# Optimization experiments

Hardware: AMD Instinct MI355X
Metric: run time of the kernel (lower is better)

The kernel has to match this reference:

```python
import jax, jax.numpy as jnp
import numpy as np

N, F, O, E = 2048, 128, 128, 16


def setup_inputs() -> dict:
    key = jax.random.key(0)
    ks = jax.random.split(key, 6)
    x = jax.random.normal(ks[0], (N, F), dtype=jnp.float32)
    # two supports (normalized adjacency-like dense matrices)
    support = jax.random.uniform(ks[1], (2, N, N), dtype=jnp.float32)
    edge_feature = jax.random.normal(ks[2], (N, N, E), dtype=jnp.float32)
    # glorot-ish scale for edge weight and dense weights
    weight_edge = jax.random.normal(ks[3], (N, N, E), dtype=jnp.float32) * 0.05
    bias_edge = jnp.zeros((N, N), dtype=jnp.float32)
    glorot = float(np.sqrt(6.0 / (F + O)))
    w0 = jax.random.uniform(ks[4], (F, O), dtype=jnp.float32, minval=-glorot, maxval=glorot)
    w1 = jax.random.uniform(ks[5], (F, O), dtype=jnp.float32, minval=-glorot, maxval=glorot)
    b = jnp.zeros((O,), dtype=jnp.float32)
    return {"x": x, "support": support, "edge_feature": edge_feature,
            "weight_edge": weight_edge, "bias_edge": bias_edge,
            "w0": w0, "w1": w1, "b": b}


def reference(x, support, edge_feature, weight_edge, bias_edge, w0, w1, b):
    # support branch 0: plain GCN propagation  (SpMM expressed dense)
    pre0 = x @ w0                      # [N, O]
    s0 = support[0] @ pre0             # [N, O]
    # support branch 1: edge-feature gated propagation
    pre1 = x @ w1                      # [N, O]
    # per-pair dot of edge features with per-pair weights -> [N, N] gate
    edge = jax.nn.sigmoid(jnp.einsum('nme,nme->nm', edge_feature, weight_edge) + bias_edge)
    s1 = (edge * support[1]) @ pre1    # gated adjacency matmul, [N, O]
    out = s0 + s1 + b                  # add_n + bias
    return jax.nn.relu(out)
```

## Files before the change

kernel.cpp:

```cpp
#include <hip/hip_runtime.h>
#include <math.h>

#define N 2048
#define F 128
#define O 128
#define E 16

typedef __attribute__((ext_vector_type(8))) short          shortx8;
typedef __attribute__((ext_vector_type(8))) unsigned short u16x8;
typedef __attribute__((ext_vector_type(4))) unsigned short u16x4;
typedef __attribute__((ext_vector_type(4))) float          floatx4;

static __device__ __forceinline__ unsigned short f2bf(float f) {
    unsigned int u = __float_as_uint(f);
    unsigned int r = (u + 0x7FFFu + ((u >> 16) & 1u)) >> 16;
    return (unsigned short)r;
}

__global__ __launch_bounds__(256)
void pre_t(const float* __restrict__ x,
           const float* __restrict__ w0,
           const float* __restrict__ w1,
           unsigned short* __restrict__ preT) {
    __shared__ unsigned short wT[128 * 136];
    const int t  = threadIdx.x;
    const int n0 = blockIdx.x * 16;
    const int b  = blockIdx.y;
    const float* __restrict__ wsrc = b ? w1 : w0;

#pragma unroll
    for (int i = 0; i < 64; ++i) {
        const int idx = i * 256 + t;
        const int k = idx >> 7, o = idx & 127;
        wT[o * 136 + k] = f2bf(wsrc[idx]);
    }
    __syncthreads();

    const int lane = t & 63;
    const int wv   = t >> 6;
    const int row  = lane & 15;
    const int kg   = lane >> 4;
    const int col0 = wv * 32 + row;

    floatx4 acc0 = {0.f, 0.f, 0.f, 0.f};
    floatx4 acc1 = {0.f, 0.f, 0.f, 0.f};

#pragma unroll
    for (int kk = 0; kk < 4; ++kk) {
        const float* xp = x + (size_t)(n0 + row) * F + kk * 32 + kg * 8;
        const float4 f0 = *(const float4*)(xp);
        const float4 f1 = *(const float4*)(xp + 4);
        shortx8 a;
        a[0] = (short)f2bf(f0.x); a[1] = (short)f2bf(f0.y);
        a[2] = (short)f2bf(f0.z); a[3] = (short)f2bf(f0.w);
        a[4] = (short)f2bf(f1.x); a[5] = (short)f2bf(f1.y);
        a[6] = (short)f2bf(f1.z); a[7] = (short)f2bf(f1.w);
        const shortx8 bA = *(const shortx8*)(wT + col0 * 136 + kk * 32 + kg * 8);
        const shortx8 bB = *(const shortx8*)(wT + (col0 + 16) * 136 + kk * 32 + kg * 8);
        acc0 = __builtin_amdgcn_mfma_f32_16x16x32_bf16(a, bA, acc0, 0, 0, 0);
        acc1 = __builtin_amdgcn_mfma_f32_16x16x32_bf16(a, bB, acc1, 0, 0, 0);
    }

    const int prow = kg * 4;
    u16x4 s0, s1;
#pragma unroll
    for (int j = 0; j < 4; ++j) { s0[j] = f2bf(acc0[j]); s1[j] = f2bf(acc1[j]); }
    *(u16x4*)(preT + ((size_t)b * O + col0) * N + n0 + prow)      = s0;
    *(u16x4*)(preT + ((size_t)b * O + col0 + 16) * N + n0 + prow) = s1;
}

__global__ __launch_bounds__(256)
void gate_kernel(const float* __restrict__ ef,
                 const float* __restrict__ we,
                 const float* __restrict__ be,
                 const float* __restrict__ sup1,
                 unsigned short* __restrict__ G) {
    const size_t tid  = (size_t)blockIdx.x * 256 + threadIdx.x;
    const size_t pair = tid >> 2;
    const int    sub  = (int)(threadIdx.x & 3);
    const float4 e4 = ((const float4*)ef)[pair * 4 + sub];
    const float4 w4 = ((const float4*)we)[pair * 4 + sub];
    float v = e4.x * w4.x + e4.y * w4.y + e4.z * w4.z + e4.w * w4.w;
    v += __shfl_xor(v, 1);
    v += __shfl_xor(v, 2);
    if (sub == 0) {
        const float t = v + be[pair];
        const float g = (1.f / (1.f + __expf(-t))) * sup1[pair];
        G[pair] = f2bf(g);
    }
}

__global__ __launch_bounds__(512, 4)
void gemm_direct(const float* __restrict__ S0,
                 const unsigned short* __restrict__ G,
                 const unsigned short* __restrict__ preT,
                 const float* __restrict__ bias,
                 float* __restrict__ out) {
    __shared__ float red[8][16][36];

    const int bx   = blockIdx.x;
    const int orig = (bx & 7) * 64 + (bx >> 3);
    const int rb   = orig >> 2;
    const int cg   = orig & 3;
    const int n0   = rb * 16;

    const int t    = threadIdx.x;
    const int lane = t & 63;
    const int wv   = t >> 6;
    const int m_b  = wv * 256;
    const int row  = lane & 15;
    const int kg   = lane >> 4;
    const int col0 = cg * 32 + row;

    const float*          aS = S0   + (size_t)(n0 + row) * N + m_b + kg * 8;
    const unsigned short* aG = G    + (size_t)(n0 + row) * N + m_b + kg * 8;
    const unsigned short* b0 = preT + (size_t)col0 * N        + m_b + kg * 8;
    const unsigned short* b1 = b0 + (size_t)16 * N;
    const unsigned short* c0 = b0 + (size_t)O * N;
    const unsigned short* c1 = b1 + (size_t)O * N;

    floatx4 acc0 = {0.f, 0.f, 0.f, 0.f};
    floatx4 acc1 = {0.f, 0.f, 0.f, 0.f};

#pragma unroll 2
    for (int s = 0; s < 8; ++s) {
        const int mo = s * 32;
        const float4 f0 = *(const float4*)(aS + mo);
        const float4 f1 = *(const float4*)(aS + mo + 4);
        const shortx8 a_g = *(const shortx8*)(aG + mo);
        const shortx8 b00 = *(const shortx8*)(b0 + mo);
        const shortx8 b01 = *(const shortx8*)(b1 + mo);
        const shortx8 b10 = *(const shortx8*)(c0 + mo);
        const shortx8 b11 = *(const shortx8*)(c1 + mo);
        shortx8 a_s;
        a_s[0] = (short)f2bf(f0.x); a_s[1] = (short)f2bf(f0.y);
        a_s[2] = (short)f2bf(f0.z); a_s[3] = (short)f2bf(f0.w);
        a_s[4] = (short)f2bf(f1.x); a_s[5] = (short)f2bf(f1.y);
        a_s[6] = (short)f2bf(f1.z); a_s[7] = (short)f2bf(f1.w);
        acc0 = __builtin_amdgcn_mfma_f32_16x16x32_bf16(a_s, b00, acc0, 0, 0, 0);
        acc0 = __builtin_amdgcn_mfma_f32_16x16x32_bf16(a_g, b10, acc0, 0, 0, 0);
        acc1 = __builtin_amdgcn_mfma_f32_16x16x32_bf16(a_s, b01, acc1, 0, 0, 0);
        acc1 = __builtin_amdgcn_mfma_f32_16x16x32_bf16(a_g, b11, acc1, 0, 0, 0);
    }

    const int prow = kg * 4;
#pragma unroll
    for (int j = 0; j < 4; ++j) {
        red[wv][prow + j][row]      = acc0[j];
        red[wv][prow + j][16 + row] = acc1[j];
    }
    __syncthreads();

    if (t < 256) {
        const int r = t >> 4;
        const int c = (t & 15) * 2;
        float v0 = 0.f, v1 = 0.f;
#pragma unroll
        for (int w = 0; w < 8; ++w) {
            v0 += red[w][r][c];
            v1 += red[w][r][c + 1];
        }
        v0 = fmaxf(v0 + bias[cg * 32 + c],     0.f);
        v1 = fmaxf(v1 + bias[cg * 32 + c + 1], 0.f);
        float2 o2; o2.x = v0; o2.y = v1;
        *(float2*)(out + (size_t)(n0 + r) * O + cg * 32 + c) = o2;
    }
}

extern "C" void kernel_launch(void* const* d_in, const int* in_sizes, int n_in,
                              void* d_out, int out_size, void* d_ws, size_t ws_size,
                              hipStream_t stream) {
    const float* x   = (const float*)d_in[0];
    const float* sup = (const float*)d_in[1];
    const float* ef  = (const float*)d_in[2];
    const float* we  = (const float*)d_in[3];
    const float* be  = (const float*)d_in[4];
    const float* w0  = (const float*)d_in[5];
    const float* w1  = (const float*)d_in[6];
    const float* b   = (const float*)d_in[7];
    float* out = (float*)d_out;

    unsigned short* preT = (unsigned short*)d_ws;
    unsigned short* G    = preT + 2 * (size_t)N * O;

    pre_t<<<dim3(N / 16, 2), 256, 0, stream>>>(x, w0, w1, preT);
    gate_kernel<<<(unsigned)((size_t)N * N * 4 / 256), 256, 0, stream>>>(
        ef, we, be, sup + (size_t)N * N, G);
    gemm_direct<<<512, 512, 0, stream>>>(sup, G, preT, b, out);
}
```

Before: 130.5 us.

## Pre-convert support0 to bf16 in gate kernel and widen GEMM to 16 waves

The gate kernel now also converts support[0] to bf16 into a workspace buffer, so the final GEMM reads half the bytes for that operand and skips in-loop conversion. The GEMM block doubles to 1024 threads, each wave covering a shorter K slice with all operand loads issued before the MFMAs. This adds an extra fp32 read and bf16 write in the bandwidth-bound gate kernel and a larger shared reduction.

```diff
diff --git a/kernel.cpp b/kernel.cpp
--- a/kernel.cpp
+++ b/kernel.cpp
@@ -74,7 +74,9 @@
                  const float* __restrict__ we,
                  const float* __restrict__ be,
                  const float* __restrict__ sup1,
-                 unsigned short* __restrict__ G) {
+                 const float* __restrict__ S0,
+                 unsigned short* __restrict__ G,
+                 unsigned short* __restrict__ S0bf) {
     const size_t tid  = (size_t)blockIdx.x * 256 + threadIdx.x;
     const size_t pair = tid >> 2;
     const int    sub  = (int)(threadIdx.x & 3);
@@ -87,16 +89,18 @@
         const float t = v + be[pair];
         const float g = (1.f / (1.f + __expf(-t))) * sup1[pair];
         G[pair] = f2bf(g);
+    } else if (sub == 1) {
+        S0bf[pair] = f2bf(S0[pair]);
     }
 }
 
-__global__ __launch_bounds__(512, 4)
-void gemm_direct(const float* __restrict__ S0,
+__global__ __launch_bounds__(1024, 4)
+void gemm_direct(const unsigned short* __restrict__ S0bf,
                  const unsigned short* __restrict__ G,
                  const unsigned short* __restrict__ preT,
                  const float* __restrict__ bias,
                  float* __restrict__ out) {
-    __shared__ float red[8][16][36];
+    __shared__ float red[16][16][36];
 
     const int bx   = blockIdx.x;
     const int orig = (bx & 7) * 64 + (bx >> 3);
@@ -107,40 +111,38 @@
     const int t    = threadIdx.x;
     const int lane = t & 63;
     const int wv   = t >> 6;
-    const int m_b  = wv * 256;
+    const int m_b  = wv * 128;
     const int row  = lane & 15;
     const int kg   = lane >> 4;
     const int col0 = cg * 32 + row;
 
-    const float*          aS = S0   + (size_t)(n0 + row) * N + m_b + kg * 8;
+    const unsigned short* aS = S0bf + (size_t)(n0 + row) * N + m_b + kg * 8;
     const unsigned short* aG = G    + (size_t)(n0 + row) * N + m_b + kg * 8;
     const unsigned short* b0 = preT + (size_t)col0 * N        + m_b + kg * 8;
     const unsigned short* b1 = b0 + (size_t)16 * N;
     const unsigned short* c0 = b0 + (size_t)O * N;
     const unsigned short* c1 = b1 + (size_t)O * N;
 
+    shortx8 As[4], Ag[4], B00[4], B01[4], B10[4], B11[4];
+#pragma unroll
+    for (int s = 0; s < 4; ++s) {
+        const int mo = s * 32;
+        As[s]  = *(const shortx8*)(aS + mo);
+        Ag[s]  = *(const shortx8*)(aG + mo);
+        B00[s] = *(const shortx8*)(b0 + mo);
+        B01[s] = *(const shortx8*)(b1 + mo);
+        B10[s] = *(const shortx8*)(c0 + mo);
+        B11[s] = *(const shortx8*)(c1 + mo);
+    }
+
     floatx4 acc0 = {0.f, 0.f, 0.f, 0.f};
     floatx4 acc1 = {0.f, 0.f, 0.f, 0.f};
-
-#pragma unroll 2
-    for (int s = 0; s < 8; ++s) {
-        const int mo = s * 32;
-        const float4 f0 = *(const float4*)(aS + mo);
-        const float4 f1 = *(const float4*)(aS + mo + 4);
-        const shortx8 a_g = *(const shortx8*)(aG + mo);
-        const shortx8 b00 = *(const shortx8*)(b0 + mo);
-        const shortx8 b01 = *(const shortx8*)(b1 + mo);
-        const shortx8 b10 = *(const shortx8*)(c0 + mo);
-        const shortx8 b11 = *(const shortx8*)(c1 + mo);
-        shortx8 a_s;
-        a_s[0] = (short)f2bf(f0.x); a_s[1] = (short)f2bf(f0.y);
-        a_s[2] = (short)f2bf(f0.z); a_s[3] = (short)f2bf(f0.w);
-        a_s[4] = (short)f2bf(f1.x); a_s[5] = (short)f2bf(f1.y);
-        a_s[6] = (short)f2bf(f1.z); a_s[7] = (short)f2bf(f1.w);
-        acc0 = __builtin_amdgcn_mfma_f32_16x16x32_bf16(a_s, b00, acc0, 0, 0, 0);
-        acc0 = __builtin_amdgcn_mfma_f32_16x16x32_bf16(a_g, b10, acc0, 0, 0, 0);
-        acc1 = __builtin_amdgcn_mfma_f32_16x16x32_bf16(a_s, b01, acc1, 0, 0, 0);
-        acc1 = __builtin_amdgcn_mfma_f32_16x16x32_bf16(a_g, b11, acc1, 0, 0, 0);
+#pragma unroll
+    for (int s = 0; s < 4; ++s) {
+        acc0 = __builtin_amdgcn_mfma_f32_16x16x32_bf16(As[s], B00[s], acc0, 0, 0, 0);
+        acc0 = __builtin_amdgcn_mfma_f32_16x16x32_bf16(Ag[s], B10[s], acc0, 0, 0, 0);
+        acc1 = __builtin_amdgcn_mfma_f32_16x16x32_bf16(As[s], B01[s], acc1, 0, 0, 0);
+        acc1 = __builtin_amdgcn_mfma_f32_16x16x32_bf16(Ag[s], B11[s], acc1, 0, 0, 0);
     }
 
     const int prow = kg * 4;
@@ -156,7 +158,7 @@
         const int c = (t & 15) * 2;
         float v0 = 0.f, v1 = 0.f;
 #pragma unroll
-        for (int w = 0; w < 8; ++w) {
+        for (int w = 0; w < 16; ++w) {
             v0 += red[w][r][c];
             v1 += red[w][r][c + 1];
         }
@@ -182,9 +184,10 @@
 
     unsigned short* preT = (unsigned short*)d_ws;
     unsigned short* G    = preT + 2 * (size_t)N * O;
+    unsigned short* S0bf = G + (size_t)N * N;
 
     pre_t<<<dim3(N / 16, 2), 256, 0, stream>>>(x, w0, w1, preT);
     gate_kernel<<<(unsigned)((size_t)N * N * 4 / 256), 256, 0, stream>>>(
-        ef, we, be, sup + (size_t)N * N, G);
-    gemm_direct<<<512, 512, 0, stream>>>(sup, G, preT, b, out);
+        ef, we, be, sup + (size_t)N * N, sup, G, S0bf);
+    gemm_direct<<<512, 1024, 0, stream>>>(S0bf, G, preT, b, out);
 }
```

New measurement: 133.0 us. About the same (+1.9%).

## Move support0 GEMM into the gate kernel to overlap with the gate pass

Applied to the files above, without the earlier changes.

Splits the support0 matmul out of the final GEMM and runs it in extra blocks at the front of the gate kernel. Those blocks write a float partial result that the final GEMM reads in its epilogue. The compute-heavy S0 work can then overlap with the memory-bound gate pass, and the final kernel only handles the gated branch. The cost is an extra partial buffer written and read, plus heterogeneous blocks inside one launch.

```diff
diff --git a/kernel.cpp b/kernel.cpp
--- a/kernel.cpp
+++ b/kernel.cpp
@@ -69,33 +69,92 @@
     *(u16x4*)(preT + ((size_t)b * O + col0 + 16) * N + n0 + prow) = s1;
 }
 
+#define S0_BLOCKS 512
+
 __global__ __launch_bounds__(256)
-void gate_kernel(const float* __restrict__ ef,
-                 const float* __restrict__ we,
-                 const float* __restrict__ be,
-                 const float* __restrict__ sup1,
-                 unsigned short* __restrict__ G) {
-    const size_t tid  = (size_t)blockIdx.x * 256 + threadIdx.x;
-    const size_t pair = tid >> 2;
-    const int    sub  = (int)(threadIdx.x & 3);
-    const float4 e4 = ((const float4*)ef)[pair * 4 + sub];
-    const float4 w4 = ((const float4*)we)[pair * 4 + sub];
-    float v = e4.x * w4.x + e4.y * w4.y + e4.z * w4.z + e4.w * w4.w;
-    v += __shfl_xor(v, 1);
-    v += __shfl_xor(v, 2);
-    if (sub == 0) {
-        const float t = v + be[pair];
-        const float g = (1.f / (1.f + __expf(-t))) * sup1[pair];
-        G[pair] = f2bf(g);
+void gate_s0(const float* __restrict__ ef,
+             const float* __restrict__ we,
+             const float* __restrict__ be,
+             const float* __restrict__ sup,
+             const unsigned short* __restrict__ preT,
+             unsigned short* __restrict__ G,
+             float* __restrict__ partial0) {
+    __shared__ float red[4][16][36];
+    const int bx = blockIdx.x;
+    const int t  = threadIdx.x;
+
+    if (bx < S0_BLOCKS) {
+        const int rb   = bx >> 2;
+        const int cg   = bx & 3;
+        const int n0   = rb * 16;
+        const int lane = t & 63;
+        const int wv   = t >> 6;
+        const int m_b  = wv * 512;
+        const int row  = lane & 15;
+        const int kg   = lane >> 4;
+        const int col0 = cg * 32 + row;
+
+        const float*          aS = sup  + (size_t)(n0 + row) * N + m_b + kg * 8;
+        const unsigned short* b0 = preT + (size_t)col0 * N       + m_b + kg * 8;
+        const unsigned short* b1 = b0 + (size_t)16 * N;
+
+        floatx4 acc0 = {0.f, 0.f, 0.f, 0.f};
+        floatx4 acc1 = {0.f, 0.f, 0.f, 0.f};
+
+#pragma unroll 2
+        for (int s = 0; s < 16; ++s) {
+            const int mo = s * 32;
+            const float4 f0 = *(const float4*)(aS + mo);
+            const float4 f1 = *(const float4*)(aS + mo + 4);
+            const shortx8 b00 = *(const shortx8*)(b0 + mo);
+            const shortx8 b01 = *(const shortx8*)(b1 + mo);
+            shortx8 a_s;
+            a_s[0] = (short)f2bf(f0.x); a_s[1] = (short)f2bf(f0.y);
+            a_s[2] = (short)f2bf(f0.z); a_s[3] = (short)f2bf(f0.w);
+            a_s[4] = (short)f2bf(f1.x); a_s[5] = (short)f2bf(f1.y);
+            a_s[6] = (short)f2bf(f1.z); a_s[7] = (short)f2bf(f1.w);
+            acc0 = __builtin_amdgcn_mfma_f32_16x16x32_bf16(a_s, b00, acc0, 0, 0, 0);
+            acc1 = __builtin_amdgcn_mfma_f32_16x16x32_bf16(a_s, b01, acc1, 0, 0, 0);
+        }
+
+        const int prow = kg * 4;
+#pragma unroll
+        for (int j = 0; j < 4; ++j) {
+            red[wv][prow + j][row]      = acc0[j];
+            red[wv][prow + j][16 + row] = acc1[j];
+        }
+        __syncthreads();
+
+        const int r = t >> 4;
+        const int c = (t & 15) * 2;
+        float v0 = red[0][r][c]     + red[1][r][c]     + red[2][r][c]     + red[3][r][c];
+        float v1 = red[0][r][c + 1] + red[1][r][c + 1] + red[2][r][c + 1] + red[3][r][c + 1];
+        float2 o2; o2.x = v0; o2.y = v1;
+        *(float2*)(partial0 + (size_t)(n0 + r) * O + cg * 32 + c) = o2;
+    } else {
+        const float* __restrict__ sup1 = sup + (size_t)N * N;
+        const size_t tid  = (size_t)(bx - S0_BLOCKS) * 256 + t;
+        const size_t pair = tid >> 2;
+        const int    sub  = t & 3;
+        const float4 e4 = ((const float4*)ef)[pair * 4 + sub];
+        const float4 w4 = ((const float4*)we)[pair * 4 + sub];
+        float v = e4.x * w4.x + e4.y * w4.y + e4.z * w4.z + e4.w * w4.w;
+        v += __shfl_xor(v, 1);
+        v += __shfl_xor(v, 2);
+        if (sub == 0) {
+            const float tt = v + be[pair];
+            const float g  = (1.f / (1.f + __expf(-tt))) * sup1[pair];
+            G[pair] = f2bf(g);
+        }
     }
 }
 
 __global__ __launch_bounds__(512, 4)
-void gemm_direct(const float* __restrict__ S0,
-                 const unsigned short* __restrict__ G,
-                 const unsigned short* __restrict__ preT,
-                 const float* __restrict__ bias,
-                 float* __restrict__ out) {
+void gemm_g_out(const unsigned short* __restrict__ G,
+                const unsigned short* __restrict__ preT,
+                const float* __restrict__ partial0,
+                const float* __restrict__ bias,
+                float* __restrict__ out) {
     __shared__ float red[8][16][36];
 
     const int bx   = blockIdx.x;
@@ -112,12 +171,9 @@
     const int kg   = lane >> 4;
     const int col0 = cg * 32 + row;
 
-    const float*          aS = S0   + (size_t)(n0 + row) * N + m_b + kg * 8;
-    const unsigned short* aG = G    + (size_t)(n0 + row) * N + m_b + kg * 8;
-    const unsigned short* b0 = preT + (size_t)col0 * N        + m_b + kg * 8;
-    const unsigned short* b1 = b0 + (size_t)16 * N;
-    const unsigned short* c0 = b0 + (size_t)O * N;
-    const unsigned short* c1 = b1 + (size_t)O * N;
+    const unsigned short* aG = G    + (size_t)(n0 + row) * N      + m_b + kg * 8;
+    const unsigned short* c0 = preT + (size_t)(O + col0) * N      + m_b + kg * 8;
+    const unsigned short* c1 = c0 + (size_t)16 * N;
 
     floatx4 acc0 = {0.f, 0.f, 0.f, 0.f};
     floatx4 acc1 = {0.f, 0.f, 0.f, 0.f};
@@ -125,21 +181,10 @@
 #pragma unroll 2
     for (int s = 0; s < 8; ++s) {
         const int mo = s * 32;
-        const float4 f0 = *(const float4*)(aS + mo);
-        const float4 f1 = *(const float4*)(aS + mo + 4);
         const shortx8 a_g = *(const shortx8*)(aG + mo);
-        const shortx8 b00 = *(const shortx8*)(b0 + mo);
-        const shortx8 b01 = *(const shortx8*)(b1 + mo);
         const shortx8 b10 = *(const shortx8*)(c0 + mo);
         const shortx8 b11 = *(const shortx8*)(c1 + mo);
-        shortx8 a_s;
-        a_s[0] = (short)f2bf(f0.x); a_s[1] = (short)f2bf(f0.y);
-        a_s[2] = (short)f2bf(f0.z); a_s[3] = (short)f2bf(f0.w);
-        a_s[4] = (short)f2bf(f1.x); a_s[5] = (short)f2bf(f1.y);
-        a_s[6] = (short)f2bf(f1.z); a_s[7] = (short)f2bf(f1.w);
-        acc0 = __builtin_amdgcn_mfma_f32_16x16x32_bf16(a_s, b00, acc0, 0, 0, 0);
         acc0 = __builtin_amdgcn_mfma_f32_16x16x32_bf16(a_g, b10, acc0, 0, 0, 0);
-        acc1 = __builtin_amdgcn_mfma_f32_16x16x32_bf16(a_s, b01, acc1, 0, 0, 0);
         acc1 = __builtin_amdgcn_mfma_f32_16x16x32_bf16(a_g, b11, acc1, 0, 0, 0);
     }
 
@@ -160,8 +205,9 @@
             v0 += red[w][r][c];
             v1 += red[w][r][c + 1];
         }
-        v0 = fmaxf(v0 + bias[cg * 32 + c],     0.f);
-        v1 = fmaxf(v1 + bias[cg * 32 + c + 1], 0.f);
+        const float2 p0 = *(const float2*)(partial0 + (size_t)(n0 + r) * O + cg * 32 + c);
+        v0 = fmaxf(v0 + p0.x + bias[cg * 32 + c],     0.f);
+        v1 = fmaxf(v1 + p0.y + bias[cg * 32 + c + 1], 0.f);
         float2 o2; o2.x = v0; o2.y = v1;
         *(float2*)(out + (size_t)(n0 + r) * O + cg * 32 + c) = o2;
     }
@@ -180,11 +226,12 @@
     const float* b   = (const float*)d_in[7];
     float* out = (float*)d_out;
 
-    unsigned short* preT = (unsigned short*)d_ws;
-    unsigned short* G    = preT + 2 * (size_t)N * O;
+    unsigned short* preT     = (unsigned short*)d_ws;
+    unsigned short* G        = preT + 2 * (size_t)N * O;
+    float*          partial0 = (float*)(G + (size_t)N * N);
 
     pre_t<<<dim3(N / 16, 2), 256, 0, stream>>>(x, w0, w1, preT);
-    gate_kernel<<<(unsigned)((size_t)N * N * 4 / 256), 256, 0, stream>>>(
-        ef, we, be, sup + (size_t)N * N, G);
-    gemm_direct<<<512, 512, 0, stream>>>(sup, G, preT, b, out);
-}
+    gate_s0<<<S0_BLOCKS + (unsigned)((size_t)N * N * 4 / 256), 256, 0, stream>>>(
+        ef, we, be, sup, preT, G, partial0);
+    gemm_g_out<<<512, 512, 0, stream>>>(G, preT, partial0, b, out);
+}
```

After: 138.6 us. 1.06x slower.
